# Optimization experiments

Measured on AMD Instinct MI355X. Metric: run time of the kernel, lower is better.

Reference implementation:

```python
import jax, jax.numpy as jnp
import numpy as np

NEG_SLOPE = 0.01  # torch LeakyReLU default
MIN_FREQ = 1.0
MAX_FREQ = 10.0
W = 100
N_HIDDEN = 100
N_OBS = 64

def _leaky(x):
    return jnp.where(x >= 0, x, NEG_SLOPE * x)

def setup_inputs() -> dict:
    key = jax.random.key(0)
    ks = jax.random.split(key, 7)
    # kaiming_uniform-ish init scales (exact init doesn't matter for correctness baseline)
    def unif(k, shape, fan_in):
        bound = np.sqrt(6.0 / fan_in)
        return jax.random.uniform(k, shape, jnp.float32, -bound, bound)
    x = jax.random.normal(ks[0], (65536, N_OBS), jnp.float32)
    W_in = unif(ks[1], (N_OBS, W), N_OBS)
    b_in = jnp.zeros((W,), jnp.float32)
    Ws = unif(ks[2], (N_HIDDEN, W, W), W)
    bs = jnp.zeros((N_HIDDEN, W), jnp.float32)
    W_out = unif(ks[3], (W, 1), W)
    b_out = jnp.zeros((1,), jnp.float32)
    return {"x": x, "W_in": W_in, "b_in": b_in, "Ws": Ws, "bs": bs,
            "W_out": W_out, "b_out": b_out}

def reference(x, W_in, b_in, Ws, bs, W_out, b_out):
    h = _leaky(x @ W_in + b_in)                       # [B, 100]
    def layer(h, wb):
        w, b = wb
        return _leaky(h @ w + b), None
    h, _ = jax.lax.scan(layer, h, (Ws, bs))           # 100 hidden layers
    a = h @ W_out + b_out                             # [B, 1]
    a = jnp.tanh(a)
    return (a + 1.0) / 2.0 * (MAX_FREQ - MIN_FREQ) + MIN_FREQ
```

## Files before the change

### kernel.cpp

```cpp
#include <hip/hip_runtime.h>
#include <cmath>

#define NLAYERS 100
#define DIN     64
#define WDIM    100
#define NTT     4
#define NTW     2
#define RT      2
#define ROWS    64
#define KS      7
#define PSTR    136
#define BUF     (64 * PSTR)

typedef _Float16 half8  __attribute__((ext_vector_type(8)));
typedef _Float16 half2v __attribute__((ext_vector_type(2)));
typedef __fp16   fp16x2 __attribute__((ext_vector_type(2)));
typedef float    f32x4  __attribute__((ext_vector_type(4)));
typedef float    f32x16 __attribute__((ext_vector_type(16)));

#define WSH_LAYER_HALVES (KS * NTT * 64 * 8)
#define WSH_HALVES       (NLAYERS * WSH_LAYER_HALVES)
#define W0_HALVES        (4 * NTT * 64 * 8)
#define BPAD_FLOATS      128
#define OFF_BPAD_B       ((WSH_HALVES + W0_HALVES) * 2)
#define OFF_WOUT_B       (OFF_BPAD_B + BPAD_FLOATS * 4)
#define WOUT_FLOATS      128
#define TOTAL_PREP       (WSH_HALVES + W0_HALVES + BPAD_FLOATS + WOUT_FLOATS)

__global__ void actor_prep(const float* __restrict__ Win, const float* __restrict__ bin,
                           const float* __restrict__ Ws,  const float* __restrict__ bs,
                           const float* __restrict__ Wout,
                           _Float16* __restrict__ wsh, _Float16* __restrict__ w0sh,
                           float* __restrict__ bpad, float* __restrict__ woutp) {
    int t = blockIdx.x * 256 + threadIdx.x;
    if (t < WSH_HALVES) {
        int j    = t & 7;
        int lane = (t >> 3) & 63;
        int fid  = t >> 9;
        int nt   = fid & 3;
        int r2   = fid >> 2;
        int ks   = r2 % 7;
        int l    = r2 / 7;
        int k = ks * 16 + (lane >> 5) * 8 + j;
        int n = nt * 32 + (lane & 31);
        float v = 0.f;
        if (k < WDIM && n < WDIM)            v = Ws[(l * WDIM + k) * WDIM + n];
        else if (k == 100 && n < WDIM)       v = bs[l * WDIM + n];
        else if (k == 100 && n == 100)       v = 1.0f;
        wsh[t] = (_Float16)v;
        return;
    }
    int t2 = t - WSH_HALVES;
    if (t2 < W0_HALVES) {
        int j    = t2 & 7;
        int lane = (t2 >> 3) & 63;
        int fid  = t2 >> 9;
        int nt   = fid & 3;
        int ks   = fid >> 2;
        int k = ks * 16 + (lane >> 5) * 8 + j;
        int n = nt * 32 + (lane & 31);
        float v = (n < WDIM) ? Win[k * WDIM + n] : 0.f;
        w0sh[t2] = (_Float16)v;
        return;
    }
    int t3 = t2 - WSH_HALVES >= 0 ? t2 - W0_HALVES : 0;
    t3 = t2 - W0_HALVES;
    if (t3 < BPAD_FLOATS) {
        float v = (t3 < WDIM) ? bin[t3] : (t3 == 100 ? 1.0f : 0.f);
        bpad[t3] = v;
        return;
    }
    int t4 = t3 - BPAD_FLOATS;
    if (t4 < WOUT_FLOATS) woutp[t4] = (t4 < WDIM) ? Wout[t4] : 0.f;
}

__device__ __forceinline__ void split8(const float* __restrict__ p, half8& hi, half8& lo) {
    f32x4 u0 = *(const f32x4*)p;
    f32x4 u1 = *(const f32x4*)(p + 4);
    float v[8] = {u0[0], u0[1], u0[2], u0[3], u1[0], u1[1], u1[2], u1[3]};
#pragma unroll
    for (int e = 0; e < 8; e += 2) {
        fp16x2 h = __builtin_amdgcn_cvt_pkrtz(v[e], v[e + 1]);
        float r0 = v[e]     - (float)h[0];
        float r1 = v[e + 1] - (float)h[1];
        fp16x2 l = __builtin_amdgcn_cvt_pkrtz(r0, r1);
        hi[e] = (_Float16)h[0]; hi[e + 1] = (_Float16)h[1];
        lo[e] = (_Float16)l[0]; lo[e + 1] = (_Float16)l[1];
    }
}

__device__ __forceinline__ void ep_quad(const f32x16 a, int qd, _Float16* __restrict__ d) {
    half2v p01, p23;
    p01[0] = (_Float16)a[4 * qd + 0]; p01[1] = (_Float16)a[4 * qd + 1];
    p23[0] = (_Float16)a[4 * qd + 2]; p23[1] = (_Float16)a[4 * qd + 3];
    const half2v slope = {(_Float16)0.01f, (_Float16)0.01f};
    p01 = __builtin_elementwise_max(p01, p01 * slope);
    p23 = __builtin_elementwise_max(p23, p23 * slope);
    uint2 w;
    w.x = __builtin_bit_cast(unsigned, p01);
    w.y = __builtin_bit_cast(unsigned, p23);
    *reinterpret_cast<uint2*>(d) = w;
}

__global__ __launch_bounds__(128, 2)
void actor_main(const float* __restrict__ x,
                const _Float16* __restrict__ wsh,
                const _Float16* __restrict__ w0sh,
                const float* __restrict__ bpad,
                const float* __restrict__ woutp,
                const float* __restrict__ bout,
                float* __restrict__ out) {
    __shared__ _Float16 hp[2 * BUF];
    const int lane = threadIdx.x & 63;
    const int wid  = threadIdx.x >> 6;
    const int g = lane >> 5, b31 = lane & 31;
    const int rowbase = blockIdx.x * ROWS;
    const int ntb = wid * NTW;

    f32x16 acc[RT][NTW];
    half8 wb[KS][NTW];
    const f32x16 zero16 = {0,0,0,0, 0,0,0,0, 0,0,0,0, 0,0,0,0};

    half8 w0[4][NTW];
#pragma unroll
    for (int ks = 0; ks < 4; ++ks)
#pragma unroll
        for (int ntl = 0; ntl < NTW; ++ntl)
            w0[ks][ntl] = *(const half8*)(w0sh + (ks * NTT + ntb + ntl) * 512 + lane * 8);
#pragma unroll
    for (int rt = 0; rt < RT; ++rt)
#pragma unroll
        for (int ntl = 0; ntl < NTW; ++ntl)
#pragma unroll
            for (int qd = 0; qd < 4; ++qd) {
                f32x4 tq = *(const f32x4*)(bpad + (ntb + ntl) * 32 + 8 * qd + 4 * g);
#pragma unroll
                for (int r = 0; r < 4; ++r) acc[rt][ntl][4 * qd + r] = tq[r];
            }
#pragma unroll
    for (int rt = 0; rt < RT; ++rt) {
        const float* xr = x + (rowbase + rt * 32 + b31) * DIN;
#pragma unroll
        for (int ks = 0; ks < 4; ++ks) {
            half8 xhi, xlo;
            split8(xr + ks * 16 + g * 8, xhi, xlo);
#pragma unroll
            for (int ntl = 0; ntl < NTW; ++ntl) {
                acc[rt][ntl] = __builtin_amdgcn_mfma_f32_32x32x16_f16(w0[ks][ntl], xhi, acc[rt][ntl], 0, 0, 0);
                acc[rt][ntl] = __builtin_amdgcn_mfma_f32_32x32x16_f16(w0[ks][ntl], xlo, acc[rt][ntl], 0, 0, 0);
            }
        }
    }
#pragma unroll
    for (int rt = 0; rt < RT; ++rt)
#pragma unroll
        for (int ntl = 0; ntl < NTW; ++ntl) {
            _Float16* d = hp + (rt * 32 + b31) * PSTR + (ntb + ntl) * 32 + 4 * g;
#pragma unroll
            for (int qd = 0; qd < 4; ++qd) ep_quad(acc[rt][ntl], qd, d + 8 * qd);
        }
#pragma unroll
    for (int ks = 0; ks < KS; ++ks)
#pragma unroll
        for (int ntl = 0; ntl < NTW; ++ntl)
            wb[ks][ntl] = *(const half8*)(wsh + (ks * NTT + ntb + ntl) * 512 + lane * 8);
    __syncthreads();

#pragma unroll 1
    for (int l = 0; l < NLAYERS; ++l) {
        const _Float16* rb = hp + (l & 1) * BUF;
        _Float16* wbf = hp + ((l + 1) & 1) * BUF;
        const _Float16* wn = wsh + (l < NLAYERS - 1 ? l + 1 : l) * WSH_LAYER_HALVES;
        half8 bh[KS];

#pragma unroll
        for (int ks = 0; ks < KS; ++ks)
            bh[ks] = *(const half8*)(rb + b31 * PSTR + ks * 16 + g * 8);
#pragma unroll
        for (int ks = 0; ks < KS; ++ks) {
            acc[0][0] = __builtin_amdgcn_mfma_f32_32x32x16_f16(
                wb[ks][0], bh[ks], (ks == 0 ? zero16 : acc[0][0]), 0, 0, 0);
            acc[0][1] = __builtin_amdgcn_mfma_f32_32x32x16_f16(
                wb[ks][1], bh[ks], (ks == 0 ? zero16 : acc[0][1]), 0, 0, 0);
        }

#pragma unroll
        for (int ks = 0; ks < KS; ++ks)
            bh[ks] = *(const half8*)(rb + (32 + b31) * PSTR + ks * 16 + g * 8);
        _Float16* d00 = wbf + b31 * PSTR + (ntb + 0) * 32 + 4 * g;
        _Float16* d01 = wbf + b31 * PSTR + (ntb + 1) * 32 + 4 * g;
#pragma unroll
        for (int ks = 0; ks < KS; ++ks) {
            acc[1][0] = __builtin_amdgcn_mfma_f32_32x32x16_f16(
                wb[ks][0], bh[ks], (ks == 0 ? zero16 : acc[1][0]), 0, 0, 0);
            acc[1][1] = __builtin_amdgcn_mfma_f32_32x32x16_f16(
                wb[ks][1], bh[ks], (ks == 0 ? zero16 : acc[1][1]), 0, 0, 0);
            wb[ks][0] = *(const half8*)(wn + (ks * NTT + ntb + 0) * 512 + lane * 8);
            wb[ks][1] = *(const half8*)(wn + (ks * NTT + ntb + 1) * 512 + lane * 8);
            if (ks < 4) {
                ep_quad(acc[0][0], ks, d00 + 8 * ks);
                ep_quad(acc[0][1], ks, d01 + 8 * ks);
            }
        }
        {
            _Float16* d10 = wbf + (32 + b31) * PSTR + (ntb + 0) * 32 + 4 * g;
            _Float16* d11 = wbf + (32 + b31) * PSTR + (ntb + 1) * 32 + 4 * g;
#pragma unroll
            for (int qd = 0; qd < 4; ++qd) {
                ep_quad(acc[1][0], qd, d10 + 8 * qd);
                ep_quad(acc[1][1], qd, d11 + 8 * qd);
            }
        }
        __syncthreads();
    }

    float part[RT];
#pragma unroll
    for (int rt = 0; rt < RT; ++rt) {
        float s = 0.f;
#pragma unroll
        for (int ntl = 0; ntl < NTW; ++ntl)
#pragma unroll
            for (int qd = 0; qd < 4; ++qd) {
                f32x4 w4 = *(const f32x4*)(woutp + (ntb + ntl) * 32 + 8 * qd + 4 * g);
#pragma unroll
                for (int r = 0; r < 4; ++r) {
                    float a = acc[rt][ntl][4 * qd + r];
                    float v = fmaxf(a, 0.01f * a);
                    s += v * w4[r];
                }
            }
        s += __shfl_xor(s, 32);
        part[rt] = s;
    }
    float* red = (float*)hp;
#pragma unroll
    for (int rt = 0; rt < RT; ++rt)
        if (lane < 32) red[wid * 64 + rt * 32 + b31] = part[rt];
    __syncthreads();
    {
        const int r = threadIdx.x;
        if (r < 64) {
            float tot = red[r] + red[64 + r] + bout[0];
            out[rowbase + r] = tanhf(tot) * 4.5f + 5.5f;
        }
    }
}

extern "C" void kernel_launch(void* const* d_in, const int* in_sizes, int n_in,
                              void* d_out, int out_size, void* d_ws, size_t ws_size,
                              hipStream_t stream) {
    const float* x    = (const float*)d_in[0];
    const float* Win  = (const float*)d_in[1];
    const float* bin  = (const float*)d_in[2];
    const float* Ws   = (const float*)d_in[3];
    const float* bs   = (const float*)d_in[4];
    const float* Wout = (const float*)d_in[5];
    const float* bout = (const float*)d_in[6];
    float* out = (float*)d_out;

    char* ws = (char*)d_ws;
    _Float16* wsh  = (_Float16*)ws;
    _Float16* w0sh = wsh + WSH_HALVES;
    float* bpad  = (float*)(ws + OFF_BPAD_B);
    float* woutp = (float*)(ws + OFF_WOUT_B);

    hipLaunchKernelGGL(actor_prep, dim3((TOTAL_PREP + 255) / 256), dim3(256), 0, stream,
                       Win, bin, Ws, bs, Wout, wsh, w0sh, bpad, woutp);

    const int nrows = in_sizes[0] / DIN;
    hipLaunchKernelGGL(actor_main, dim3(nrows / ROWS), dim3(128), 0, stream,
                       x, wsh, w0sh, bpad, woutp, bout, out);
}
```

Before: 255.1 us.

## Split N-tiles across four waves, swizzle LDS, coalesce weight prep via shared tile

The main kernel goes from 2 waves each handling two 32-column N tiles to 4 waves each handling one, which halves per-wave accumulators and weight registers and raises occupancy. LDS activation reads and writes use an XOR swizzle to reduce bank conflicts. The layer barrier becomes an inline s_waitcnt plus s_barrier. The prep kernel now stages each weight tile through shared memory so global reads are coalesced and writes are 16-byte vectors. In exchange, more waves share the same LDS buffers and every wave rereads the full activation tile, raising LDS read traffic.

New measurement: 276.3 us. 8.3% more time.

```diff
diff --git a/kernel.cpp b/kernel.cpp
--- a/kernel.cpp
+++ b/kernel.cpp
@@ -5,7 +5,6 @@
 #define DIN     64
 #define WDIM    100
 #define NTT     4
-#define NTW     2
 #define RT      2
 #define ROWS    64
 #define KS      7
@@ -25,53 +24,62 @@
 #define OFF_BPAD_B       ((WSH_HALVES + W0_HALVES) * 2)
 #define OFF_WOUT_B       (OFF_BPAD_B + BPAD_FLOATS * 4)
 #define WOUT_FLOATS      128
-#define TOTAL_PREP       (WSH_HALVES + W0_HALVES + BPAD_FLOATS + WOUT_FLOATS)
-
-__global__ void actor_prep(const float* __restrict__ Win, const float* __restrict__ bin,
-                           const float* __restrict__ Ws,  const float* __restrict__ bs,
-                           const float* __restrict__ Wout,
-                           _Float16* __restrict__ wsh, _Float16* __restrict__ w0sh,
-                           float* __restrict__ bpad, float* __restrict__ woutp) {
-    int t = blockIdx.x * 256 + threadIdx.x;
-    if (t < WSH_HALVES) {
-        int j    = t & 7;
-        int lane = (t >> 3) & 63;
-        int fid  = t >> 9;
-        int nt   = fid & 3;
-        int r2   = fid >> 2;
-        int ks   = r2 % 7;
-        int l    = r2 / 7;
-        int k = ks * 16 + (lane >> 5) * 8 + j;
-        int n = nt * 32 + (lane & 31);
-        float v = 0.f;
-        if (k < WDIM && n < WDIM)            v = Ws[(l * WDIM + k) * WDIM + n];
-        else if (k == 100 && n < WDIM)       v = bs[l * WDIM + n];
-        else if (k == 100 && n == 100)       v = 1.0f;
-        wsh[t] = (_Float16)v;
+
+__global__ __launch_bounds__(256)
+void actor_prep(const float* __restrict__ Win, const float* __restrict__ bin,
+                const float* __restrict__ Ws,  const float* __restrict__ bs,
+                const float* __restrict__ Wout,
+                _Float16* __restrict__ wsh, _Float16* __restrict__ w0sh,
+                float* __restrict__ bpad, float* __restrict__ woutp) {
+    __shared__ float tile[16 * 128];
+    const int bid = blockIdx.x, tid = threadIdx.x;
+    if (bid < NLAYERS * KS) {
+        const int l = bid / KS, ks = bid % KS;
+#pragma unroll
+        for (int e = 0; e < 8; ++e) {
+            int idx = tid + 256 * e;
+            int kk = idx >> 7, nn = idx & 127;
+            int k = ks * 16 + kk;
+            float v = 0.f;
+            if (k < WDIM && nn < WDIM)        v = Ws[(l * WDIM + k) * WDIM + nn];
+            else if (k == WDIM && nn < WDIM)  v = bs[l * WDIM + nn];
+            else if (k == WDIM && nn == WDIM) v = 1.0f;
+            tile[idx] = v;
+        }
+        __syncthreads();
+        const int lane = tid & 63, nt = tid >> 6;
+        const int g = lane >> 5, n = nt * 32 + (lane & 31);
+        half8 o;
+#pragma unroll
+        for (int j = 0; j < 8; ++j) o[j] = (_Float16)tile[(g * 8 + j) * 128 + n];
+        *(half8*)(wsh + (((l * KS + ks) * NTT + nt) << 9) + lane * 8) = o;
         return;
     }
-    int t2 = t - WSH_HALVES;
-    if (t2 < W0_HALVES) {
-        int j    = t2 & 7;
-        int lane = (t2 >> 3) & 63;
-        int fid  = t2 >> 9;
-        int nt   = fid & 3;
-        int ks   = fid >> 2;
-        int k = ks * 16 + (lane >> 5) * 8 + j;
-        int n = nt * 32 + (lane & 31);
-        float v = (n < WDIM) ? Win[k * WDIM + n] : 0.f;
-        w0sh[t2] = (_Float16)v;
+    int b2 = bid - NLAYERS * KS;
+    if (b2 < 4) {
+        const int ks = b2;
+#pragma unroll
+        for (int e = 0; e < 8; ++e) {
+            int idx = tid + 256 * e;
+            int kk = idx >> 7, nn = idx & 127;
+            int k = ks * 16 + kk;
+            tile[idx] = (nn < WDIM) ? Win[k * WDIM + nn] : 0.f;
+        }
+        __syncthreads();
+        const int lane = tid & 63, nt = tid >> 6;
+        const int g = lane >> 5, n = nt * 32 + (lane & 31);
+        half8 o;
+#pragma unroll
+        for (int j = 0; j < 8; ++j) o[j] = (_Float16)tile[(g * 8 + j) * 128 + n];
+        *(half8*)(w0sh + ((ks * NTT + nt) << 9) + lane * 8) = o;
         return;
     }
-    int t3 = t2 - WSH_HALVES >= 0 ? t2 - W0_HALVES : 0;
-    t3 = t2 - W0_HALVES;
-    if (t3 < BPAD_FLOATS) {
-        float v = (t3 < WDIM) ? bin[t3] : (t3 == 100 ? 1.0f : 0.f);
-        bpad[t3] = v;
-        return;
-    }
-    int t4 = t3 - BPAD_FLOATS;
-    if (t4 < WOUT_FLOATS) woutp[t4] = (t4 < WDIM) ? Wout[t4] : 0.f;
+    if (tid < BPAD_FLOATS) {
+        bpad[tid] = (tid < WDIM) ? bin[tid] : (tid == WDIM ? 1.0f : 0.f);
+    } else {
+        int t = tid - BPAD_FLOATS;
+        if (t < WOUT_FLOATS) woutp[t] = (t < WDIM) ? Wout[t] : 0.f;
+    }
 }
 
 __device__ __forceinline__ void split8(const float* __restrict__ p, half8& hi, half8& lo) {
@@ -102,7 +110,7 @@
     *reinterpret_cast<uint2*>(d) = w;
 }
 
-__global__ __launch_bounds__(128, 2)
+__global__ __launch_bounds__(256, 4)
 void actor_main(const float* __restrict__ x,
                 const _Float16* __restrict__ wsh,
                 const _Float16* __restrict__ w0sh,
@@ -110,61 +118,52 @@
                 const float* __restrict__ woutp,
                 const float* __restrict__ bout,
                 float* __restrict__ out) {
-    __shared__ _Float16 hp[2 * BUF];
+    __shared__ __align__(16) _Float16 hp[2 * BUF];
     const int lane = threadIdx.x & 63;
     const int wid  = threadIdx.x >> 6;
     const int g = lane >> 5, b31 = lane & 31;
+    const int sw = ((b31 >> 3) & 1) << 5;
     const int rowbase = blockIdx.x * ROWS;
-    const int ntb = wid * NTW;
-
-    f32x16 acc[RT][NTW];
-    half8 wb[KS][NTW];
+
+    f32x16 acc[RT];
+    half8 wb[KS];
     const f32x16 zero16 = {0,0,0,0, 0,0,0,0, 0,0,0,0, 0,0,0,0};
 
-    half8 w0[4][NTW];
-#pragma unroll
-    for (int ks = 0; ks < 4; ++ks)
-#pragma unroll
-        for (int ntl = 0; ntl < NTW; ++ntl)
-            w0[ks][ntl] = *(const half8*)(w0sh + (ks * NTT + ntb + ntl) * 512 + lane * 8);
-#pragma unroll
-    for (int rt = 0; rt < RT; ++rt)
-#pragma unroll
-        for (int ntl = 0; ntl < NTW; ++ntl)
+    {
+        half8 w0[4];
+#pragma unroll
+        for (int ks = 0; ks < 4; ++ks)
+            w0[ks] = *(const half8*)(w0sh + (ks * NTT + wid) * 512 + lane * 8);
+#pragma unroll
+        for (int rt = 0; rt < RT; ++rt)
 #pragma unroll
             for (int qd = 0; qd < 4; ++qd) {
-                f32x4 tq = *(const f32x4*)(bpad + (ntb + ntl) * 32 + 8 * qd + 4 * g);
-#pragma unroll
-                for (int r = 0; r < 4; ++r) acc[rt][ntl][4 * qd + r] = tq[r];
+                f32x4 tq = *(const f32x4*)(bpad + wid * 32 + 8 * qd + 4 * g);
+#pragma unroll
+                for (int r = 0; r < 4; ++r) acc[rt][4 * qd + r] = tq[r];
             }
 #pragma unroll
+        for (int rt = 0; rt < RT; ++rt) {
+            const float* xr = x + (rowbase + rt * 32 + b31) * DIN;
+#pragma unroll
+            for (int ks = 0; ks < 4; ++ks) {
+                half8 xhi, xlo;
+                split8(xr + ks * 16 + g * 8, xhi, xlo);
+                acc[rt] = __builtin_amdgcn_mfma_f32_32x32x16_f16(w0[ks], xhi, acc[rt], 0, 0, 0);
+                acc[rt] = __builtin_amdgcn_mfma_f32_32x32x16_f16(w0[ks], xlo, acc[rt], 0, 0, 0);
+            }
+        }
+    }
+#pragma unroll
     for (int rt = 0; rt < RT; ++rt) {
-        const float* xr = x + (rowbase + rt * 32 + b31) * DIN;
-#pragma unroll
-        for (int ks = 0; ks < 4; ++ks) {
-            half8 xhi, xlo;
-            split8(xr + ks * 16 + g * 8, xhi, xlo);
-#pragma unroll
-            for (int ntl = 0; ntl < NTW; ++ntl) {
-                acc[rt][ntl] = __builtin_amdgcn_mfma_f32_32x32x16_f16(w0[ks][ntl], xhi, acc[rt][ntl], 0, 0, 0);
-                acc[rt][ntl] = __builtin_amdgcn_mfma_f32_32x32x16_f16(w0[ks][ntl], xlo, acc[rt][ntl], 0, 0, 0);
-            }
-        }
-    }
-#pragma unroll
-    for (int rt = 0; rt < RT; ++rt)
-#pragma unroll
-        for (int ntl = 0; ntl < NTW; ++ntl) {
-            _Float16* d = hp + (rt * 32 + b31) * PSTR + (ntb + ntl) * 32 + 4 * g;
-#pragma unroll
-            for (int qd = 0; qd < 4; ++qd) ep_quad(acc[rt][ntl], qd, d + 8 * qd);
-        }
+        _Float16* d = hp + (rt * 32 + b31) * PSTR + ((wid * 32 + 4 * g) ^ sw);
+#pragma unroll
+        for (int qd = 0; qd < 4; ++qd) ep_quad(acc[rt], qd, d + 8 * qd);
+    }
 #pragma unroll
     for (int ks = 0; ks < KS; ++ks)
-#pragma unroll
-        for (int ntl = 0; ntl < NTW; ++ntl)
-            wb[ks][ntl] = *(const half8*)(wsh + (ks * NTT + ntb + ntl) * 512 + lane * 8);
-    __syncthreads();
+        wb[ks] = *(const half8*)(wsh + (ks * NTT + wid) * 512 + lane * 8);
+    asm volatile("s_waitcnt lgkmcnt(0)\n\ts_barrier" ::: "memory");
 
 #pragma unroll 1
     for (int l = 0; l < NLAYERS; ++l) {
@@ -175,43 +174,30 @@
 
 #pragma unroll
         for (int ks = 0; ks < KS; ++ks)
-            bh[ks] = *(const half8*)(rb + b31 * PSTR + ks * 16 + g * 8);
+            bh[ks] = *(const half8*)(rb + b31 * PSTR + ((ks * 16 + g * 8) ^ sw));
+#pragma unroll
+        for (int ks = 0; ks < KS; ++ks)
+            acc[0] = __builtin_amdgcn_mfma_f32_32x32x16_f16(
+                wb[ks], bh[ks], (ks == 0 ? zero16 : acc[0]), 0, 0, 0);
+
+#pragma unroll
+        for (int ks = 0; ks < KS; ++ks)
+            bh[ks] = *(const half8*)(rb + (32 + b31) * PSTR + ((ks * 16 + g * 8) ^ sw));
+        _Float16* d0 = wbf + b31 * PSTR + ((wid * 32 + 4 * g) ^ sw);
 #pragma unroll
         for (int ks = 0; ks < KS; ++ks) {
-            acc[0][0] = __builtin_amdgcn_mfma_f32_32x32x16_f16(
-                wb[ks][0], bh[ks], (ks == 0 ? zero16 : acc[0][0]), 0, 0, 0);
-            acc[0][1] = __builtin_amdgcn_mfma_f32_32x32x16_f16(
-                wb[ks][1], bh[ks], (ks == 0 ? zero16 : acc[0][1]), 0, 0, 0);
-        }
-
-#pragma unroll
-        for (int ks = 0; ks < KS; ++ks)
-            bh[ks] = *(const half8*)(rb + (32 + b31) * PSTR + ks * 16 + g * 8);
-        _Float16* d00 = wbf + b31 * PSTR + (ntb + 0) * 32 + 4 * g;
-        _Float16* d01 = wbf + b31 * PSTR + (ntb + 1) * 32 + 4 * g;
-#pragma unroll
-        for (int ks = 0; ks < KS; ++ks) {
-            acc[1][0] = __builtin_amdgcn_mfma_f32_32x32x16_f16(
-                wb[ks][0], bh[ks], (ks == 0 ? zero16 : acc[1][0]), 0, 0, 0);
-            acc[1][1] = __builtin_amdgcn_mfma_f32_32x32x16_f16(
-                wb[ks][1], bh[ks], (ks == 0 ? zero16 : acc[1][1]), 0, 0, 0);
-            wb[ks][0] = *(const half8*)(wn + (ks * NTT + ntb + 0) * 512 + lane * 8);
-            wb[ks][1] = *(const half8*)(wn + (ks * NTT + ntb + 1) * 512 + lane * 8);
-            if (ks < 4) {
-                ep_quad(acc[0][0], ks, d00 + 8 * ks);
-                ep_quad(acc[0][1], ks, d01 + 8 * ks);
-            }
+            acc[1] = __builtin_amdgcn_mfma_f32_32x32x16_f16(
+                wb[ks], bh[ks], (ks == 0 ? zero16 : acc[1]), 0, 0, 0);
+            wb[ks] = *(const half8*)(wn + (ks * NTT + wid) * 512 + lane * 8);
+            if (ks < 4)
+                ep_quad(acc[0], ks, d0 + 8 * ks);
         }
         {
-            _Float16* d10 = wbf + (32 + b31) * PSTR + (ntb + 0) * 32 + 4 * g;
-            _Float16* d11 = wbf + (32 + b31) * PSTR + (ntb + 1) * 32 + 4 * g;
-#pragma unroll
-            for (int qd = 0; qd < 4; ++qd) {
-                ep_quad(acc[1][0], qd, d10 + 8 * qd);
-                ep_quad(acc[1][1], qd, d11 + 8 * qd);
-            }
-        }
-        __syncthreads();
+            _Float16* d1 = wbf + (32 + b31) * PSTR + ((wid * 32 + 4 * g) ^ sw);
+#pragma unroll
+            for (int qd = 0; qd < 4; ++qd) ep_quad(acc[1], qd, d1 + 8 * qd);
+        }
+        asm volatile("s_waitcnt lgkmcnt(0)\n\ts_barrier" ::: "memory");
     }
 
     float part[RT];
@@ -219,29 +205,28 @@
     for (int rt = 0; rt < RT; ++rt) {
         float s = 0.f;
 #pragma unroll
-        for (int ntl = 0; ntl < NTW; ++ntl)
-#pragma unroll
-            for (int qd = 0; qd < 4; ++qd) {
-                f32x4 w4 = *(const f32x4*)(woutp + (ntb + ntl) * 32 + 8 * qd + 4 * g);
-#pragma unroll
-                for (int r = 0; r < 4; ++r) {
-                    float a = acc[rt][ntl][4 * qd + r];
-                    float v = fmaxf(a, 0.01f * a);
-                    s += v * w4[r];
-                }
+        for (int qd = 0; qd < 4; ++qd) {
+            f32x4 w4 = *(const f32x4*)(woutp + wid * 32 + 8 * qd + 4 * g);
+#pragma unroll
+            for (int r = 0; r < 4; ++r) {
+                float a = acc[rt][4 * qd + r];
+                float v = fmaxf(a, 0.01f * a);
+                s += v * w4[r];
             }
+        }
         s += __shfl_xor(s, 32);
         part[rt] = s;
     }
     float* red = (float*)hp;
-#pragma unroll
-    for (int rt = 0; rt < RT; ++rt)
-        if (lane < 32) red[wid * 64 + rt * 32 + b31] = part[rt];
+    if (lane < 32) {
+        red[wid * 64 + b31]      = part[0];
+        red[wid * 64 + 32 + b31] = part[1];
+    }
     __syncthreads();
     {
         const int r = threadIdx.x;
         if (r < 64) {
-            float tot = red[r] + red[64 + r] + bout[0];
+            float tot = red[r] + red[64 + r] + red[128 + r] + red[192 + r] + bout[0];
             out[rowbase + r] = tanhf(tot) * 4.5f + 5.5f;
         }
     }
@@ -265,10 +250,10 @@
     float* bpad  = (float*)(ws + OFF_BPAD_B);
     float* woutp = (float*)(ws + OFF_WOUT_B);
 
-    hipLaunchKernelGGL(actor_prep, dim3((TOTAL_PREP + 255) / 256), dim3(256), 0, stream,
+    hipLaunchKernelGGL(actor_prep, dim3(NLAYERS * KS + 4 + 1), dim3(256), 0, stream,
                        Win, bin, Ws, bs, Wout, wsh, w0sh, bpad, woutp);
 
     const int nrows = in_sizes[0] / DIN;
-    hipLaunchKernelGGL(actor_main, dim3(nrows / ROWS), dim3(128), 0, stream,
+    hipLaunchKernelGGL(actor_main, dim3(nrows / ROWS), dim3(256), 0, stream,
                        x, wsh, w0sh, bpad, woutp, bout, out);
 }
```
